# Kernel tuning notes

Hardware: AMD Instinct MI355X
Metric: run time of the kernel (lower is better)

Reference implementation:

```python
import jax, jax.numpy as jnp
import numpy as np

B, N = 128, 1024


def setup_inputs() -> dict:
    key = jax.random.key(0)
    k1, k2 = jax.random.split(key)
    vector = jax.random.uniform(k1, (B, N), dtype=jnp.float32)
    interactions = jax.random.normal(k2, (N, N), dtype=jnp.float32)
    return {"vector": vector, "interactions": interactions}


def reference(vector, interactions):
    # x: [B,1,N], y: [B,N,1] -> broadcast dirac delta [B,N,N]
    x = vector[:, None, :]
    y = vector[:, :, None]
    dd = (1.0 - x) * (1.0 - y) + x * y  # [B,N,N]
    dd = jnp.triu(dd)                   # keep upper triangle incl. diagonal
    energy = dd * interactions          # [B,N,N] * [N,N] broadcast
    return energy.reshape(vector.shape[0], -1).sum(axis=1)  # [B]
```

## Files before the change

### kernel.cpp

```cpp
#include <hip/hip_runtime.h>

#define NDIM 1024
#define BDIM 128
#define NB 4
#define NGRP (BDIM / NB)
#define NPH 16
#define RPW 16

__global__ __launch_bounds__(256) void potts_single(
    const float* __restrict__ V,
    const float* __restrict__ W,
    float* __restrict__ out)
{
    const int g = blockIdx.x;
    const int bg = g & (NGRP - 1);
    const int phase = g >> 5;
    const int b0 = bg * NB;

    const int tid = threadIdx.x;
    const int w = tid >> 6;
    const int l = tid & 63;

    __shared__ float4 lq[4][RPW];
    __shared__ float4 lr[4][RPW];
    __shared__ float4 redw[4];

    float4 vj[NB][4];
#pragma unroll
    for (int bb = 0; bb < NB; ++bb) {
        const float* vb = V + (size_t)(b0 + bb) * NDIM;
#pragma unroll
        for (int c = 0; c < 4; ++c)
            vj[bb][c] = *(const float4*)(vb + 256 * c + 4 * l);
    }

    if (tid < 64) {
        const int w2 = tid & 3, ii = tid >> 2;
        const int i = 64 * ii + 4 * phase + w2;
        const float v0 = V[(size_t)(b0 + 0) * NDIM + i];
        const float v1 = V[(size_t)(b0 + 1) * NDIM + i];
        const float v2 = V[(size_t)(b0 + 2) * NDIM + i];
        const float v3 = V[(size_t)(b0 + 3) * NDIM + i];
        lq[w2][ii] = make_float4(1.f - v0, 1.f - v1, 1.f - v2, 1.f - v3);
        lr[w2][ii] = make_float4(2.f * v0 - 1.f, 2.f * v1 - 1.f,
                                 2.f * v2 - 1.f, 2.f * v3 - 1.f);
    }
    __syncthreads();

    float acc0 = 0.f, acc1 = 0.f, acc2 = 0.f, acc3 = 0.f;

#pragma unroll 2
    for (int ii = 0; ii < RPW; ++ii) {
        const int i = 64 * ii + 4 * phase + w;
        const float* wrow = W + (size_t)i * NDIM;
        float s0 = 0.f, s1a = 0.f, s1b = 0.f, s1c = 0.f, s1d = 0.f;
#pragma unroll
        for (int c = 0; c < 4; ++c) {
            if (256 * c + 255 >= i) {
                const int j0 = 256 * c + 4 * l;
                if (j0 + 3 >= i) {
                    float4 w4 = *(const float4*)(wrow + j0);
                    const int d = i - j0;
                    if (d > 0) {
                        w4.x = 0.f;
                        if (d > 1) w4.y = 0.f;
                        if (d > 2) w4.z = 0.f;
                    }
                    s0 += (w4.x + w4.y) + (w4.z + w4.w);
                    s1a = fmaf(w4.x, vj[0][c].x, s1a);
                    s1a = fmaf(w4.y, vj[0][c].y, s1a);
                    s1a = fmaf(w4.z, vj[0][c].z, s1a);
                    s1a = fmaf(w4.w, vj[0][c].w, s1a);
                    s1b = fmaf(w4.x, vj[1][c].x, s1b);
                    s1b = fmaf(w4.y, vj[1][c].y, s1b);
                    s1b = fmaf(w4.z, vj[1][c].z, s1b);
                    s1b = fmaf(w4.w, vj[1][c].w, s1b);
                    s1c = fmaf(w4.x, vj[2][c].x, s1c);
                    s1c = fmaf(w4.y, vj[2][c].y, s1c);
                    s1c = fmaf(w4.z, vj[2][c].z, s1c);
                    s1c = fmaf(w4.w, vj[2][c].w, s1c);
                    s1d = fmaf(w4.x, vj[3][c].x, s1d);
                    s1d = fmaf(w4.y, vj[3][c].y, s1d);
                    s1d = fmaf(w4.z, vj[3][c].z, s1d);
                    s1d = fmaf(w4.w, vj[3][c].w, s1d);
                }
            }
        }
        const float4 q = lq[w][ii];
        const float4 r = lr[w][ii];
        acc0 = fmaf(q.x, s0, acc0); acc0 = fmaf(r.x, s1a, acc0);
        acc1 = fmaf(q.y, s0, acc1); acc1 = fmaf(r.y, s1b, acc1);
        acc2 = fmaf(q.z, s0, acc2); acc2 = fmaf(r.z, s1c, acc2);
        acc3 = fmaf(q.w, s0, acc3); acc3 = fmaf(r.w, s1d, acc3);
    }

#pragma unroll
    for (int off = 32; off > 0; off >>= 1) {
        acc0 += __shfl_down(acc0, off);
        acc1 += __shfl_down(acc1, off);
        acc2 += __shfl_down(acc2, off);
        acc3 += __shfl_down(acc3, off);
    }
    if (l == 0) redw[w] = make_float4(acc0, acc1, acc2, acc3);
    __syncthreads();
    if (tid < NB) {
        const float* rp = (const float*)redw;
        const float s = (rp[tid] + rp[4 + tid]) + (rp[8 + tid] + rp[12 + tid]);
        atomicAdd(&out[b0 + tid], s);
    }
}

extern "C" void kernel_launch(void* const* d_in, const int* in_sizes, int n_in,
                              void* d_out, int out_size, void* d_ws, size_t ws_size,
                              hipStream_t stream) {
    const float* V = (const float*)d_in[0];
    const float* W = (const float*)d_in[1];
    float* out = (float*)d_out;

    potts_single<<<dim3(NGRP * NPH), dim3(256), 0, stream>>>(V, W, out);
}
```

Baseline: 74.16 us.

## Process eight batch rows per block and mask triangle with selects

```diff
diff --git a/kernel.cpp b/kernel.cpp
--- a/kernel.cpp
+++ b/kernel.cpp
@@ -2,28 +2,38 @@
 
 #define NDIM 1024
 #define BDIM 128
-#define NB 4
+#define NB 8
 #define NGRP (BDIM / NB)
-#define NPH 16
-#define RPW 16
+#define NPH 32
+#define RPW 8
 
-__global__ __launch_bounds__(256) void potts_single(
+__global__ __launch_bounds__(256, 2) void potts_v9(
     const float* __restrict__ V,
     const float* __restrict__ W,
     float* __restrict__ out)
 {
     const int g = blockIdx.x;
     const int bg = g & (NGRP - 1);
-    const int phase = g >> 5;
+    const int ph = g >> 4;
     const int b0 = bg * NB;
 
     const int tid = threadIdx.x;
     const int w = tid >> 6;
     const int l = tid & 63;
 
-    __shared__ float4 lq[4][RPW];
-    __shared__ float4 lr[4][RPW];
-    __shared__ float4 redw[4];
+    __shared__ float lq[4][RPW][NB];
+    __shared__ float lr[4][RPW][NB];
+    __shared__ float red[4][NB];
+
+    {
+        const int bb = tid >> 5;
+        const int k  = tid & 31;
+        const int ww = k & 3, ii = k >> 2;
+        const int i = 128 * ii + 4 * ph + ww;
+        const float v = V[(size_t)(b0 + bb) * NDIM + i];
+        lq[ww][ii][bb] = 1.0f - v;
+        lr[ww][ii][bb] = 2.0f * v - 1.0f;
+    }
 
     float4 vj[NB][4];
 #pragma unroll
@@ -33,79 +43,63 @@
         for (int c = 0; c < 4; ++c)
             vj[bb][c] = *(const float4*)(vb + 256 * c + 4 * l);
     }
-
-    if (tid < 64) {
-        const int w2 = tid & 3, ii = tid >> 2;
-        const int i = 64 * ii + 4 * phase + w2;
-        const float v0 = V[(size_t)(b0 + 0) * NDIM + i];
-        const float v1 = V[(size_t)(b0 + 1) * NDIM + i];
-        const float v2 = V[(size_t)(b0 + 2) * NDIM + i];
-        const float v3 = V[(size_t)(b0 + 3) * NDIM + i];
-        lq[w2][ii] = make_float4(1.f - v0, 1.f - v1, 1.f - v2, 1.f - v3);
-        lr[w2][ii] = make_float4(2.f * v0 - 1.f, 2.f * v1 - 1.f,
-                                 2.f * v2 - 1.f, 2.f * v3 - 1.f);
-    }
     __syncthreads();
 
-    float acc0 = 0.f, acc1 = 0.f, acc2 = 0.f, acc3 = 0.f;
+    float acc[NB];
+#pragma unroll
+    for (int bb = 0; bb < NB; ++bb) acc[bb] = 0.0f;
 
 #pragma unroll 2
     for (int ii = 0; ii < RPW; ++ii) {
-        const int i = 64 * ii + 4 * phase + w;
+        const int i = 128 * ii + 4 * ph + w;
         const float* wrow = W + (size_t)i * NDIM;
-        float s0 = 0.f, s1a = 0.f, s1b = 0.f, s1c = 0.f, s1d = 0.f;
+        float s0 = 0.0f;
+        float s1[NB];
+#pragma unroll
+        for (int bb = 0; bb < NB; ++bb) s1[bb] = 0.0f;
+
 #pragma unroll
         for (int c = 0; c < 4; ++c) {
-            if (256 * c + 255 >= i) {
-                const int j0 = 256 * c + 4 * l;
-                if (j0 + 3 >= i) {
-                    float4 w4 = *(const float4*)(wrow + j0);
-                    const int d = i - j0;
-                    if (d > 0) {
-                        w4.x = 0.f;
-                        if (d > 1) w4.y = 0.f;
-                        if (d > 2) w4.z = 0.f;
-                    }
-                    s0 += (w4.x + w4.y) + (w4.z + w4.w);
-                    s1a = fmaf(w4.x, vj[0][c].x, s1a);
-                    s1a = fmaf(w4.y, vj[0][c].y, s1a);
-                    s1a = fmaf(w4.z, vj[0][c].z, s1a);
-                    s1a = fmaf(w4.w, vj[0][c].w, s1a);
-                    s1b = fmaf(w4.x, vj[1][c].x, s1b);
-                    s1b = fmaf(w4.y, vj[1][c].y, s1b);
-                    s1b = fmaf(w4.z, vj[1][c].z, s1b);
-                    s1b = fmaf(w4.w, vj[1][c].w, s1b);
-                    s1c = fmaf(w4.x, vj[2][c].x, s1c);
-                    s1c = fmaf(w4.y, vj[2][c].y, s1c);
-                    s1c = fmaf(w4.z, vj[2][c].z, s1c);
-                    s1c = fmaf(w4.w, vj[2][c].w, s1c);
-                    s1d = fmaf(w4.x, vj[3][c].x, s1d);
-                    s1d = fmaf(w4.y, vj[3][c].y, s1d);
-                    s1d = fmaf(w4.z, vj[3][c].z, s1d);
-                    s1d = fmaf(w4.w, vj[3][c].w, s1d);
-                }
+            const int j0 = 256 * c + 4 * l;
+            float4 w4 = *(const float4*)(wrow + j0);
+            w4.x = (j0 + 0 >= i) ? w4.x : 0.0f;
+            w4.y = (j0 + 1 >= i) ? w4.y : 0.0f;
+            w4.z = (j0 + 2 >= i) ? w4.z : 0.0f;
+            w4.w = (j0 + 3 >= i) ? w4.w : 0.0f;
+            s0 += (w4.x + w4.y) + (w4.z + w4.w);
+#pragma unroll
+            for (int bb = 0; bb < NB; ++bb) {
+                s1[bb] = fmaf(w4.x, vj[bb][c].x, s1[bb]);
+                s1[bb] = fmaf(w4.y, vj[bb][c].y, s1[bb]);
+                s1[bb] = fmaf(w4.z, vj[bb][c].z, s1[bb]);
+                s1[bb] = fmaf(w4.w, vj[bb][c].w, s1[bb]);
             }
         }
-        const float4 q = lq[w][ii];
-        const float4 r = lr[w][ii];
-        acc0 = fmaf(q.x, s0, acc0); acc0 = fmaf(r.x, s1a, acc0);
-        acc1 = fmaf(q.y, s0, acc1); acc1 = fmaf(r.y, s1b, acc1);
-        acc2 = fmaf(q.z, s0, acc2); acc2 = fmaf(r.z, s1c, acc2);
-        acc3 = fmaf(q.w, s0, acc3); acc3 = fmaf(r.w, s1d, acc3);
+        const float4 q0 = *(const float4*)(&lq[w][ii][0]);
+        const float4 q1 = *(const float4*)(&lq[w][ii][4]);
+        const float4 r0 = *(const float4*)(&lr[w][ii][0]);
+        const float4 r1 = *(const float4*)(&lr[w][ii][4]);
+        acc[0] = fmaf(q0.x, s0, acc[0]); acc[0] = fmaf(r0.x, s1[0], acc[0]);
+        acc[1] = fmaf(q0.y, s0, acc[1]); acc[1] = fmaf(r0.y, s1[1], acc[1]);
+        acc[2] = fmaf(q0.z, s0, acc[2]); acc[2] = fmaf(r0.z, s1[2], acc[2]);
+        acc[3] = fmaf(q0.w, s0, acc[3]); acc[3] = fmaf(r0.w, s1[3], acc[3]);
+        acc[4] = fmaf(q1.x, s0, acc[4]); acc[4] = fmaf(r1.x, s1[4], acc[4]);
+        acc[5] = fmaf(q1.y, s0, acc[5]); acc[5] = fmaf(r1.y, s1[5], acc[5]);
+        acc[6] = fmaf(q1.z, s0, acc[6]); acc[6] = fmaf(r1.z, s1[6], acc[6]);
+        acc[7] = fmaf(q1.w, s0, acc[7]); acc[7] = fmaf(r1.w, s1[7], acc[7]);
     }
 
 #pragma unroll
-    for (int off = 32; off > 0; off >>= 1) {
-        acc0 += __shfl_down(acc0, off);
-        acc1 += __shfl_down(acc1, off);
-        acc2 += __shfl_down(acc2, off);
-        acc3 += __shfl_down(acc3, off);
+    for (int bb = 0; bb < NB; ++bb) {
+        float a = acc[bb];
+#pragma unroll
+        for (int off = 32; off > 0; off >>= 1)
+            a += __shfl_down(a, off);
+        if (l == 0) red[w][bb] = a;
     }
-    if (l == 0) redw[w] = make_float4(acc0, acc1, acc2, acc3);
     __syncthreads();
     if (tid < NB) {
-        const float* rp = (const float*)redw;
-        const float s = (rp[tid] + rp[4 + tid]) + (rp[8 + tid] + rp[12 + tid]);
+        const float s = (red[0][tid] + red[1][tid]) + (red[2][tid] + red[3][tid]);
         atomicAdd(&out[b0 + tid], s);
     }
 }
@@ -117,5 +111,5 @@
     const float* W = (const float*)d_in[1];
     float* out = (float*)d_out;
 
-    potts_single<<<dim3(NGRP * NPH), dim3(256), 0, stream>>>(V, W, out);
+    potts_v9<<<dim3(NGRP * NPH), dim3(256), 0, stream>>>(V, W, out);
 }
```

Result: faster. 68.65 us (-7.4%).
